# Kernel optimization log

Hardware: AMD Instinct MI355X
Metric: run time of the kernel (lower is better)

## Reference

```python
import jax, jax.numpy as jnp
import numpy as np

S, B, H, L = 1024, 128, 1024, 2
D = 2 * H  # concat dim: hidden + input (input_size == hidden_size)


def setup_inputs() -> dict:
    key = jax.random.key(0)
    k1, k2, k3 = jax.random.split(key, 3)
    inputs = jax.random.normal(k1, (S, B, H), dtype=jnp.float32)
    lim = 1.0 / np.sqrt(D)  # torch Linear default init range
    W = jax.random.uniform(k2, (L, 4, D), jnp.float32, -lim, lim)  # rows: i, c~, f, o
    b = jax.random.uniform(k3, (L, 4), jnp.float32, -lim, lim)
    return {"inputs": inputs, "W": W, "b": b}


def _lstm(inputs, W, b):
    Ln = W.shape[0]
    Bn, Hd = inputs.shape[1], inputs.shape[2]
    h0 = jnp.zeros((Ln, Bn, Hd), inputs.dtype)
    c0 = jnp.zeros_like(h0)

    def step(carry, x_t):
        h, c = carry  # each [L, B, H]
        inp = x_t     # [B, H]
        hs, cs = [], []
        for l in range(Ln):
            z = jnp.concatenate([h[l], inp], axis=-1)  # [B, 2H], order [H_t_1, X_t]
            g = z @ W[l].T + b[l]                       # [B, 4] — four 1-out Linears fused
            i_t = jax.nn.sigmoid(g[:, 0:1])
            c_hat = jnp.tanh(g[:, 1:2])
            f_t = jax.nn.sigmoid(g[:, 2:3])
            o_t = jax.nn.sigmoid(g[:, 3:4])
            c_new = f_t * c[l] + i_t * c_hat            # scalar gates broadcast over [B, H]
            h_new = o_t * jnp.tanh(c_new)
            hs.append(h_new)
            cs.append(c_new)
            inp = h_new
        h = jnp.stack(hs)
        c = jnp.stack(cs)
        return (h, c), h[-1]

    (hT, cT), outs = jax.lax.scan(step, (h0, c0), inputs)
    return outs, hT, cT  # outs: [S, B, H]


def reference(inputs, W, b):
    outs, hT, cT = _lstm(inputs, W, b)
    return (outs, (hT, cT))
```

## Files before the change

### kernel.cpp

```cpp
#include <hip/hip_runtime.h>

#define SS 1024
#define BB 128
#define HH 1024
#define LL 2
#define DD 2048
#define NROWS (SS*BB)
#define TSEG 512
#define NSEG 2
#define ROWSEG (TSEG*BB)
#define RPW 8
#define NSCANB 16
#define NWORKB 2048
#define L2E  1.4426950408889634f

typedef float f32x4 __attribute__((ext_vector_type(4)));

__device__ __forceinline__ float fast_rcp(float x)  { return __builtin_amdgcn_rcpf(x); }
__device__ __forceinline__ float exp2_(float x)     { return __builtin_amdgcn_exp2f(x); }

template<int CTRL>
__device__ __forceinline__ float qperm(float x){
    return __int_as_float(__builtin_amdgcn_update_dpp(0, __float_as_int(x), CTRL, 0xF, 0xF, true));
}
__device__ __forceinline__ float rowshr4(float x){
    return __int_as_float(__builtin_amdgcn_update_dpp(0, __float_as_int(x), 0x114, 0xF, 0xF, true));
}

__global__ __launch_bounds__(256) void fused_phase(
    const float* __restrict__ x, const float* __restrict__ W,
    const float* __restrict__ bias, float* out,
    float* __restrict__ s_out, float* __restrict__ finals,
    float* __restrict__ sums, float* __restrict__ state,
    int s1, int s2, int s3, int fin)
{
    float* pre = out + (size_t)NROWS * HH;
    const int tid = threadIdx.x;

    if (blockIdx.x < NSCANB) {
        if (tid >= 64) return;
        const int lane = tid;

        if (s2 < 0) {
            if (blockIdx.x == 0 && s1 == 0) {
                for (int s = 0; s < 12; ++s) {
                    const int base = (s < 4) ? s*DD
                                   : (s < 8) ? 4*DD + (s-4)*DD
                                             : 4*DD + (s-8)*DD + HH;
                    float v = 0.f;
                    #pragma unroll
                    for (int k = 0; k < 16; ++k) v += W[base + lane + k*64];
                    #pragma unroll
                    for (int off = 32; off >= 1; off >>= 1) v += __shfl_xor(v, off, 64);
                    if (lane == 0) sums[s] = v;
                }
            }
            return;
        }

        const int gate = lane & 3;
        const int L    = (lane >> 2) & 1;
        const int lb   = lane >> 3;
        const int bb   = blockIdx.x * 8 + lb;

        const float sh = sums[L*4 + gate];
        const float sx = sums[8 + gate];
        const float sc  = (gate == 1) ? (2.0f*L2E) : (-L2E);
        const float s_h = sh * sc;
        const float sxc = L ? sx * sc : 0.0f;
        const float pcc = L ? bias[4+gate] * sc : 0.0f;
        const float Ac  = (gate == 1) ? 1.0f : 0.0f;
        const float Bc  = (gate == 0) ? (2.0f*L2E) : ((gate == 1) ? -2.0f : 1.0f);

        const float* pbase = pre + ((size_t)bb << 12) + gate;
        float* obase = s_out + bb;

        const int t_lo = s2 * TSEG, t_hi = t_lo + TSEG;

        float h, cp, h0d1, h0d2;
        float4* st = (float4*)state + blockIdx.x*64 + lane;
        if (t_lo == 0) { h = 0.f; cp = 0.f; h0d1 = 0.f; h0d2 = 0.f; }
        else { float4 s = *st; h = s.x; cp = s.y; h0d1 = s.z; h0d2 = s.w; }

        constexpr int PF = 16;
        float buf[PF];
        #pragma unroll
        for (int u = 0; u < PF; ++u) buf[u] = pbase[(size_t)(t_lo + u) * 4];

        for (int t0 = t_lo; t0 < t_hi; t0 += PF) {
            #pragma unroll
            for (int u = 0; u < PF; ++u) {
                const int t = t0 + u;
                const float p = L ? pcc : buf[u];
                int tn = t + PF; if (tn > t_hi-1) tn = t_hi-1;
                buf[u] = pbase[(size_t)tn * 4];

                const float P = fmaf(h0d2, sxc, p);
                const float g = fmaf(h, s_h, P);
                const float v = fmaf(Bc, fast_rcp(1.0f + exp2_(g)), Ac);
                const float w = v * qperm<0xB1>(v);
                const float cpn = fmaf(qperm<0xAA>(v), cp, qperm<0x00>(w));
                const float th = fmaf(-2.0f, fast_rcp(1.0f + exp2_(cpn)), 1.0f);
                const float hn = qperm<0xFF>(v) * th;
                const bool disc = (u < 2) && (t0 == t_lo) && L;
                h  = disc ? h  : hn;
                cp = disc ? cp : cpn;
                h0d2 = h0d1;
                h0d1 = rowshr4(h);
                if (L && t >= t_lo + 2) obase[(size_t)(t-2) * BB] = h;
            }
        }

        const float h0f = h, c0f = cp;

        #pragma unroll
        for (int fs = 0; fs < 2; ++fs) {
            const float p = L ? pcc : buf[0];
            const float P = fmaf(h0d2, sxc, p);
            const float g = fmaf(h, s_h, P);
            const float v = fmaf(Bc, fast_rcp(1.0f + exp2_(g)), Ac);
            const float w = v * qperm<0xB1>(v);
            const float cpn = fmaf(qperm<0xAA>(v), cp, qperm<0x00>(w));
            const float th = fmaf(-2.0f, fast_rcp(1.0f + exp2_(cpn)), 1.0f);
            const float hn = qperm<0xFF>(v) * th;
            if (L) { h = hn; cp = cpn; obase[(size_t)(t_hi-2+fs) * BB] = hn; }
            h0d2 = h0d1;
        }

        *st = make_float4(h, cp, h0d1, h0d2);

        if (t_hi == SS && gate == 0) {
            if (L) { finals[128+bb] = h;   finals[384+bb] = cp  * (0.5f/L2E); }
            else   { finals[bb]     = h0f; finals[256+bb] = c0f * (0.5f/L2E); }
        }
        return;
    }

    const int lane = tid & 63;
    const int gw   = (blockIdx.x - NSCANB)*4 + (tid >> 6);

    if (s1 >= 0) {
        float4 wv[4][4];
        #pragma unroll
        for (int j = 0; j < 4; ++j)
            #pragma unroll
            for (int it = 0; it < 4; ++it)
                wv[j][it] = *(const float4*)(W + j*DD + HH + it*256 + lane*4);
        const float4 b0 = *(const float4*)(bias);

        #pragma unroll 2
        for (int j = 0; j < RPW; ++j) {
            const int row = s1*ROWSEG + gw*RPW + j;
            const float* xr = x + (size_t)row * HH;
            float a0 = 0.f, a1 = 0.f, a2 = 0.f, a3 = 0.f;
            #pragma unroll
            for (int it = 0; it < 4; ++it) {
                f32x4 xv = __builtin_nontemporal_load((const f32x4*)xr + it*64 + lane);
                a0 = fmaf(xv.x, wv[0][it].x, fmaf(xv.y, wv[0][it].y, fmaf(xv.z, wv[0][it].z, fmaf(xv.w, wv[0][it].w, a0))));
                a1 = fmaf(xv.x, wv[1][it].x, fmaf(xv.y, wv[1][it].y, fmaf(xv.z, wv[1][it].z, fmaf(xv.w, wv[1][it].w, a1))));
                a2 = fmaf(xv.x, wv[2][it].x, fmaf(xv.y, wv[2][it].y, fmaf(xv.z, wv[2][it].z, fmaf(xv.w, wv[2][it].w, a2))));
                a3 = fmaf(xv.x, wv[3][it].x, fmaf(xv.y, wv[3][it].y, fmaf(xv.z, wv[3][it].z, fmaf(xv.w, wv[3][it].w, a3))));
            }
            #pragma unroll
            for (int off = 32; off >= 1; off >>= 1) {
                a0 += __shfl_xor(a0, off, 64);
                a1 += __shfl_xor(a1, off, 64);
                a2 += __shfl_xor(a2, off, 64);
                a3 += __shfl_xor(a3, off, 64);
            }
            if (lane == 0) {
                float4 r = make_float4((a0 + b0.x) * (-L2E),
                                       (a1 + b0.y) * ( 2.0f * L2E),
                                       (a2 + b0.z) * (-L2E),
                                       (a3 + b0.w) * (-L2E));
                const int b = row & (BB-1), t = row >> 7;
                *(float4*)(pre + (((size_t)b << 10) + t) * 4) = r;
            }
        }
    }

    if (s3 >= 0) {
        const int r0 = s3*ROWSEG + gw*RPW;
        const float4 v0 = *(const float4*)(s_out + r0);
        const float4 v1 = *(const float4*)(s_out + r0 + 4);
        const float vs[RPW] = {v0.x, v0.y, v0.z, v0.w, v1.x, v1.y, v1.z, v1.w};
        #pragma unroll
        for (int j = 0; j < RPW; ++j) {
            const f32x4 vv = {vs[j], vs[j], vs[j], vs[j]};
            f32x4* dst = (f32x4*)(out + (size_t)(r0 + j) * HH);
            #pragma unroll
            for (int it = 0; it < 4; ++it)
                __builtin_nontemporal_store(vv, dst + it*64 + lane);
        }
    }

    if (fin && gw < 512) {
        const float v = finals[gw];
        const f32x4 vv = {v, v, v, v};
        f32x4* dst = (f32x4*)(out + (size_t)(NROWS + gw) * HH);
        #pragma unroll
        for (int it = 0; it < 4; ++it)
            __builtin_nontemporal_store(vv, dst + it*64 + lane);
    }
}

extern "C" void kernel_launch(void* const* d_in, const int* in_sizes, int n_in,
                              void* d_out, int out_size, void* d_ws, size_t ws_size,
                              hipStream_t stream) {
    const float* x    = (const float*)d_in[0];
    const float* W    = (const float*)d_in[1];
    const float* bias = (const float*)d_in[2];
    float* out = (float*)d_out;

    float* s_out  = (float*)d_ws;
    float* finals = s_out + NROWS;
    float* sums   = finals + 512;
    float* state  = sums + 16;

    for (int p = 0; p < 4; ++p) {
        const int a1 = (p <= 1) ? p : -1;
        const int a2 = (p >= 1 && p <= 2) ? p - 1 : -1;
        const int a3 = (p >= 2) ? p - 2 : -1;
        const int fn = (p == 3) ? 1 : 0;
        hipLaunchKernelGGL(fused_phase, dim3(NSCANB + NWORKB), dim3(256), 0, stream,
                           x, W, bias, out, s_out, finals, sums, state,
                           a1, a2, a3, fn);
    }
}
```

Measured before the change: 244.7 us.

## Store scan outputs batch-major as float4 and batch-load 64-step precomputed gates

The scan stage now writes its per-step hidden scalars into a batch-major staging buffer, packing four timesteps into one float4 store from a single lane. Previously every step did a strided scalar store. Precomputed gate values are now loaded in chunks of 64 steps instead of through a rolling 16-entry prefetch. The broadcast stage reads the new layout and scatters each value to its [t,b] output row. The intent is to cut store traffic on the serial critical path, at the cost of more registers and less coalesced output writes.

```diff
diff --git a/kernel.cpp b/kernel.cpp
--- a/kernel.cpp
+++ b/kernel.cpp
@@ -73,7 +73,7 @@
         const float Bc  = (gate == 0) ? (2.0f*L2E) : ((gate == 1) ? -2.0f : 1.0f);
 
         const float* pbase = pre + ((size_t)bb << 12) + gate;
-        float* obase = s_out + bb;
+        float* so = s_out + (size_t)bb * SS;
 
         const int t_lo = s2 * TSEG, t_hi = t_lo + TSEG;
 
@@ -82,19 +82,17 @@
         if (t_lo == 0) { h = 0.f; cp = 0.f; h0d1 = 0.f; h0d2 = 0.f; }
         else { float4 s = *st; h = s.x; cp = s.y; h0d1 = s.z; h0d2 = s.w; }
 
-        constexpr int PF = 16;
-        float buf[PF];
-        #pragma unroll
-        for (int u = 0; u < PF; ++u) buf[u] = pbase[(size_t)(t_lo + u) * 4];
-
-        for (int t0 = t_lo; t0 < t_hi; t0 += PF) {
-            #pragma unroll
-            for (int u = 0; u < PF; ++u) {
-                const int t = t0 + u;
-                const float p = L ? pcc : buf[u];
-                int tn = t + PF; if (tn > t_hi-1) tn = t_hi-1;
-                buf[u] = pbase[(size_t)tn * 4];
-
+        float hb0 = 0.f, hb1 = 0.f, hb2 = 0.f, hb3 = 0.f;
+
+        float buf[64];
+        for (int ch = 0; ch < TSEG/64; ++ch) {
+            const int tc = t_lo + ch*64;
+            #pragma unroll
+            for (int uu = 0; uu < 64; ++uu)
+                buf[uu] = pbase[(size_t)(tc + uu) * 4];
+            #pragma unroll
+            for (int uu = 0; uu < 64; ++uu) {
+                const float p = L ? pcc : buf[uu];
                 const float P = fmaf(h0d2, sxc, p);
                 const float g = fmaf(h, s_h, P);
                 const float v = fmaf(Bc, fast_rcp(1.0f + exp2_(g)), Ac);
@@ -102,12 +100,19 @@
                 const float cpn = fmaf(qperm<0xAA>(v), cp, qperm<0x00>(w));
                 const float th = fmaf(-2.0f, fast_rcp(1.0f + exp2_(cpn)), 1.0f);
                 const float hn = qperm<0xFF>(v) * th;
-                const bool disc = (u < 2) && (t0 == t_lo) && L;
+                const bool disc = (ch == 0) && (uu < 2) && L;
                 h  = disc ? h  : hn;
                 cp = disc ? cp : cpn;
                 h0d2 = h0d1;
                 h0d1 = rowshr4(h);
-                if (L && t >= t_lo + 2) obase[(size_t)(t-2) * BB] = h;
+
+                if (((uu+2)&3)==0) hb0 = h;
+                else if (((uu+2)&3)==1) hb1 = h;
+                else if (((uu+2)&3)==2) hb2 = h;
+                else hb3 = h;
+                if (((uu&3)==1) && (ch > 0 || uu >= 5) && L && gate == 0) {
+                    *(float4*)(so + tc + uu - 5) = make_float4(hb0,hb1,hb2,hb3);
+                }
             }
         }
 
@@ -115,7 +120,7 @@
 
         #pragma unroll
         for (int fs = 0; fs < 2; ++fs) {
-            const float p = L ? pcc : buf[0];
+            const float p = L ? pcc : buf[63];
             const float P = fmaf(h0d2, sxc, p);
             const float g = fmaf(h, s_h, P);
             const float v = fmaf(Bc, fast_rcp(1.0f + exp2_(g)), Ac);
@@ -123,9 +128,12 @@
             const float cpn = fmaf(qperm<0xAA>(v), cp, qperm<0x00>(w));
             const float th = fmaf(-2.0f, fast_rcp(1.0f + exp2_(cpn)), 1.0f);
             const float hn = qperm<0xFF>(v) * th;
-            if (L) { h = hn; cp = cpn; obase[(size_t)(t_hi-2+fs) * BB] = hn; }
+            if (L) { h = hn; cp = cpn;
+                     if (fs == 0) hb2 = hn; else hb3 = hn; }
             h0d2 = h0d1;
         }
+        if (L && gate == 0)
+            *(float4*)(so + t_hi - 4) = make_float4(hb0,hb1,hb2,hb3);
 
         *st = make_float4(h, cp, h0d1, h0d2);
 
@@ -180,17 +188,21 @@
     }
 
     if (s3 >= 0) {
-        const int r0 = s3*ROWSEG + gw*RPW;
-        const float4 v0 = *(const float4*)(s_out + r0);
-        const float4 v1 = *(const float4*)(s_out + r0 + 4);
-        const float vs[RPW] = {v0.x, v0.y, v0.z, v0.w, v1.x, v1.y, v1.z, v1.w};
-        #pragma unroll
-        for (int j = 0; j < RPW; ++j) {
-            const f32x4 vv = {vs[j], vs[j], vs[j], vs[j]};
-            f32x4* dst = (f32x4*)(out + (size_t)(r0 + j) * HH);
-            #pragma unroll
-            for (int it = 0; it < 4; ++it)
-                __builtin_nontemporal_store(vv, dst + it*64 + lane);
+        #pragma unroll
+        for (int rep = 0; rep < 2; ++rep) {
+            const int g  = gw*2 + rep;
+            const int b  = g >> 7;
+            const int t0 = s3*TSEG + (g & 127)*4;
+            float4 v4 = *(const float4*)(s_out + (size_t)b*SS + t0);
+            #pragma unroll
+            for (int jj = 0; jj < 4; ++jj) {
+                const float vb = (jj==0) ? v4.x : (jj==1) ? v4.y : (jj==2) ? v4.z : v4.w;
+                const f32x4 vv = {vb, vb, vb, vb};
+                f32x4* dst = (f32x4*)(out + ((size_t)(t0+jj)*BB + b) * HH);
+                #pragma unroll
+                for (int it = 0; it < 4; ++it)
+                    __builtin_nontemporal_store(vv, dst + it*64 + lane);
+            }
         }
     }
 
```

Measured after the change: 234.2 us, median of 4. 4.3% less time.
